# Kernel tuning notes

Measured on AMD Instinct MI355X. Metric: run time of the kernel, lower is better.

Reference implementation:

```python
import jax, jax.numpy as jnp
import numpy as np

IN_CHANNELS = 8
CHANNELS = 8
MASK_OUT_STRIDE = 4
N_IMGS, H, W = 2, 128, 192
N_INST = 256
WEIGHT_NUMS = [(IN_CHANNELS + 2) * CHANNELS, CHANNELS * CHANNELS, CHANNELS * 1]  # [80, 64, 8]
BIAS_NUMS = [CHANNELS, CHANNELS, 1]
NUM_GEN_PARAMS = sum(WEIGHT_NUMS) + sum(BIAS_NUMS)  # 169


def setup_inputs() -> dict:
    key = jax.random.key(0)
    k1, k2, k3, k4, k5 = jax.random.split(key, 5)
    mask_feats = jax.random.normal(k1, (N_IMGS, IN_CHANNELS, H, W), dtype=jnp.float32)
    mask_head_params = jax.random.normal(k2, (N_INST, NUM_GEN_PARAMS), dtype=jnp.float32) * 0.1
    # instance center locations in image coordinates (stride-8 map covers 1024x1536 px)
    instance_locations = jax.random.uniform(k3, (N_INST, 2), dtype=jnp.float32) * jnp.array([W * 8.0, H * 8.0])
    soi = jnp.array([64.0, 128.0, 256.0, 512.0, 1024.0], dtype=jnp.float32)
    im_inds = jax.random.randint(k4, (N_INST,), 0, N_IMGS, dtype=jnp.int32)
    fpn_levels = jax.random.randint(k5, (N_INST,), 0, 5, dtype=jnp.int32)
    return {
        "mask_feats": mask_feats,
        "mask_head_params": mask_head_params,
        "instance_locations": instance_locations,
        "soi": soi,
        "im_inds": im_inds,
        "fpn_levels": fpn_levels,
        "mask_feat_stride": 8,
    }


def compute_locations(h, w, stride):
    shifts_x = jnp.arange(w, dtype=jnp.float32) * stride + stride // 2
    shifts_y = jnp.arange(h, dtype=jnp.float32) * stride + stride // 2
    ys, xs = jnp.meshgrid(shifts_y, shifts_x, indexing="ij")
    return jnp.stack([xs.ravel(), ys.ravel()], axis=1)  # [H*W, 2] (x, y)


def _interp_axis(x, size_in, factor, axis):
    # align_corners=True resize from (size_in+1) samples to (size_in*factor+1):
    # src coordinate of output i is exactly i / factor.
    idx = jnp.arange(size_in * factor + 1)
    i0 = idx // factor
    frac = ((idx % factor).astype(x.dtype)) / factor
    a = jnp.take(x, i0, axis=axis)
    b = jnp.take(x, jnp.minimum(i0 + 1, size_in), axis=axis)
    shape = [1] * x.ndim
    shape[axis] = -1
    f = frac.reshape(shape)
    return a * (1 - f) + b * f


def aligned_bilinear(t, factor):
    # Faithful to AdelaiDet aligned_bilinear: replicate-pad (0,1,0,1), bilinear
    # align_corners=True to (h*f+1, w*f+1), replicate-pad (f//2, 0) top/left, crop.
    if factor == 1:
        return t
    n, c, h, w = t.shape
    t = jnp.pad(t, ((0, 0), (0, 0), (0, 1), (0, 1)), mode="edge")
    t = _interp_axis(t, h, factor, 2)
    t = _interp_axis(t, w, factor, 3)
    p = factor // 2
    t = jnp.pad(t, ((0, 0), (0, 0), (p, 0), (p, 0)), mode="edge")
    return t[:, :, : h * factor, : w * factor]


def reference(mask_feats, mask_head_params, instance_locations, soi, im_inds, fpn_levels, mask_feat_stride):
    n_inst = mask_head_params.shape[0]
    _, c_in, h, w = mask_feats.shape
    hw = h * w

    # relative coordinates, normalized by size-of-interest per FPN level
    locations = compute_locations(h, w, mask_feat_stride)  # [HW, 2]
    rel = instance_locations[:, None, :] - locations[None, :, :]  # [n, HW, 2]
    rel = jnp.transpose(rel, (0, 2, 1))  # [n, 2, HW]
    rel = rel / soi[fpn_levels][:, None, None]
    rel = rel.astype(mask_feats.dtype)

    feats = mask_feats[im_inds].reshape(n_inst, c_in, hw)  # [n, C, HW]
    x = jnp.concatenate([rel, feats], axis=1)  # [n, C+2, HW]

    # parse dynamic params
    splits = np.cumsum(WEIGHT_NUMS + BIAS_NUMS)[:-1]
    w0, w1, w2, b0, b1, b2 = jnp.split(mask_head_params, splits, axis=1)
    w0 = w0.reshape(n_inst, CHANNELS, c_in + 2)
    w1 = w1.reshape(n_inst, CHANNELS, CHANNELS)
    w2 = w2.reshape(n_inst, 1, CHANNELS)

    # grouped 1x1 conv stack == per-instance batched matmul + bias (+ReLU)
    x = jax.nn.relu(jnp.einsum("noi,nip->nop", w0, x) + b0[:, :, None])
    x = jax.nn.relu(jnp.einsum("noi,nip->nop", w1, x) + b1[:, :, None])
    x = jnp.einsum("noi,nip->nop", w2, x) + b2[:, :, None]  # [n, 1, HW]

    logits = x.reshape(n_inst, 1, h, w)
    factor = mask_feat_stride // MASK_OUT_STRIDE
    return aligned_bilinear(logits, factor)  # [n, 1, h*factor, w*factor]
```

## Files before the change

kernel.cpp:

```cpp
#include <hip/hip_runtime.h>


#define HI 128
#define WI 192
#define HW_ (HI * WI)
#define NP 169
#define NOUT_W 384
#define NOUT_H 256
#define LOGITS_BYTES (256u * (unsigned)HW_ * 4u)

__global__ __launch_bounds__(256, 4) void mlp_kernel(
    const float* __restrict__ feats,
    const float* __restrict__ params,
    const float* __restrict__ locs,
    const float* __restrict__ soi,
    const int*   __restrict__ im_inds,
    const int*   __restrict__ lvls,
    float*       __restrict__ logits)
{
    const int b     = blockIdx.x;
    const int n     = b / 24;
    const int chunk = b - n * 24;
    const int t     = threadIdx.x;
    const int p     = chunk * 1024 + (t << 2);

    const int   im    = im_inds[n];
    const float s     = soi[lvls[n]];
    const float inv_s = 1.0f / s;
    const float* __restrict__ P = params + n * NP;
    const float* __restrict__ F = feats + im * (8 * HW_);

    const float step = 8.0f * inv_s;
    const float ax   = (locs[2 * n + 0] - 4.0f) * inv_s;
    const float ay   = (locs[2 * n + 1] - 4.0f) * inv_s;

    const int py  = p / WI;
    const int px0 = p - py * WI;
    const float ry  = ay - (float)py * step;
    const float rx0 = ax - (float)px0 * step;
    const float rx[4] = {rx0, rx0 - step, rx0 - 2.0f * step, rx0 - 3.0f * step};

    float fv[8][4];
    #pragma unroll
    for (int k = 0; k < 8; ++k) {
        const float4 v = *reinterpret_cast<const float4*>(F + k * HW_ + p);
        fv[k][0] = v.x; fv[k][1] = v.y; fv[k][2] = v.z; fv[k][3] = v.w;
    }

    float h0[8][4];
    #pragma unroll
    for (int o = 0; o < 8; ++o) {
        const float base = fmaf(P[o * 10 + 1], ry, P[152 + o]);
        const float wx   = P[o * 10 + 0];
        #pragma unroll
        for (int j = 0; j < 4; ++j) h0[o][j] = fmaf(wx, rx[j], base);
        #pragma unroll
        for (int k = 0; k < 8; ++k) {
            const float w = P[o * 10 + 2 + k];
            #pragma unroll
            for (int j = 0; j < 4; ++j) h0[o][j] = fmaf(w, fv[k][j], h0[o][j]);
        }
        #pragma unroll
        for (int j = 0; j < 4; ++j) h0[o][j] = fmaxf(h0[o][j], 0.0f);
    }

    float h1[8][4];
    #pragma unroll
    for (int o = 0; o < 8; ++o) {
        const float bb = P[160 + o];
        #pragma unroll
        for (int j = 0; j < 4; ++j) h1[o][j] = bb;
        #pragma unroll
        for (int i = 0; i < 8; ++i) {
            const float w = P[80 + o * 8 + i];
            #pragma unroll
            for (int j = 0; j < 4; ++j) h1[o][j] = fmaf(w, h0[i][j], h1[o][j]);
        }
        #pragma unroll
        for (int j = 0; j < 4; ++j) h1[o][j] = fmaxf(h1[o][j], 0.0f);
    }

    float lg[4];
    const float b2 = P[168];
    #pragma unroll
    for (int j = 0; j < 4; ++j) lg[j] = b2;
    #pragma unroll
    for (int i = 0; i < 8; ++i) {
        const float w = P[144 + i];
        #pragma unroll
        for (int j = 0; j < 4; ++j) lg[j] = fmaf(w, h1[i][j], lg[j]);
    }

    float4 st; st.x = lg[0]; st.y = lg[1]; st.z = lg[2]; st.w = lg[3];
    *reinterpret_cast<float4*>(logits + n * HW_ + p) = st;
}

__global__ __launch_bounds__(256, 4) void upsample_kernel(
    const float* __restrict__ logits,
    float*       __restrict__ out)
{
    const int b  = blockIdx.x;
    const int n  = b >> 2;
    const int qq = b & 3;
    const int t  = threadIdx.x;
    const int Y0 = qq << 6;

    const float* __restrict__ Lg = logits + n * HW_;
    float* __restrict__ O = out + n * (NOUT_H * NOUT_W) + Y0 * NOUT_W;

    for (int g = t; g < 3072; g += 256) {
        const int yq = g / 48;
        const int c  = g - yq * 48;
        const int y  = Y0 + yq;
        const int iy2 = (y == 0) ? 0 : (y - 1);
        const int ry0 = iy2 >> 1;
        const int fy  = iy2 & 1;
        const int j0  = c << 2;
        const int jm  = (c == 0) ? 0 : (j0 - 1);

        const float* row0 = Lg + ry0 * WI;
        float4 v  = *reinterpret_cast<const float4*>(row0 + j0);
        float  vm = row0[jm];
        if (fy) {
            const float* row1 = Lg + min(ry0 + 1, HI - 1) * WI;
            const float4 w  = *reinterpret_cast<const float4*>(row1 + j0);
            const float  wm = row1[jm];
            v.x = 0.5f * (v.x + w.x); v.y = 0.5f * (v.y + w.y);
            v.z = 0.5f * (v.z + w.z); v.w = 0.5f * (v.w + w.w);
            vm  = 0.5f * (vm + wm);
        }
        float4 r0, r1;
        r0.x = 0.5f * (vm + v.x);  r0.y = v.x;
        r0.z = 0.5f * (v.x + v.y); r0.w = v.y;
        r1.x = 0.5f * (v.y + v.z); r1.y = v.z;
        r1.z = 0.5f * (v.z + v.w); r1.w = v.w;

        float* o8 = O + (g << 3);
        *reinterpret_cast<float4*>(o8)     = r0;
        *reinterpret_cast<float4*>(o8 + 4) = r1;
    }
}

__global__ __launch_bounds__(512, 4) void dynmask_fused(
    const float* __restrict__ feats, const float* __restrict__ params,
    const float* __restrict__ locs, const float* __restrict__ soi,
    const int* __restrict__ im_inds, const int* __restrict__ lvls,
    float* __restrict__ out)
{
    __shared__ __align__(16) float L[33 * WI];
    const int b  = blockIdx.x;
    const int n  = b >> 2;
    const int qq = b & 3;
    const int t  = threadIdx.x;
    const int R0 = (qq == 0) ? 0 : (32 * qq - 1);

    const int   im    = im_inds[n];
    const float s     = soi[lvls[n]];
    const float inv_s = 1.0f / s;
    const float* __restrict__ P = params + n * NP;
    const float* __restrict__ F = feats + im * (8 * HW_);
    const float step = 8.0f * inv_s;
    const float ax   = (locs[2 * n + 0] - 4.0f) * inv_s;
    const float ay   = (locs[2 * n + 1] - 4.0f) * inv_s;

    for (int idx = t; idx < 3168; idx += 512) {
        const int r   = idx / 96;
        const int c2  = idx - r * 96;
        const int py  = R0 + r;
        const int px0 = c2 * 2;
        const int gp  = py * WI + px0;
        const float ry  = ay - (float)py * step;
        const float rx0 = ax - (float)px0 * step;
        const float rx[2] = {rx0, rx0 - step};

        float fv[8][2];
        #pragma unroll
        for (int k = 0; k < 8; ++k) {
            const float2 v = *reinterpret_cast<const float2*>(F + k * HW_ + gp);
            fv[k][0] = v.x; fv[k][1] = v.y;
        }
        float h0[8][2];
        #pragma unroll
        for (int o = 0; o < 8; ++o) {
            const float base = fmaf(P[o * 10 + 1], ry, P[152 + o]);
            #pragma unroll
            for (int j = 0; j < 2; ++j) h0[o][j] = fmaf(P[o * 10 + 0], rx[j], base);
            #pragma unroll
            for (int k = 0; k < 8; ++k)
                #pragma unroll
                for (int j = 0; j < 2; ++j) h0[o][j] = fmaf(P[o * 10 + 2 + k], fv[k][j], h0[o][j]);
            #pragma unroll
            for (int j = 0; j < 2; ++j) h0[o][j] = fmaxf(h0[o][j], 0.0f);
        }
        float h1[8][2];
        #pragma unroll
        for (int o = 0; o < 8; ++o) {
            #pragma unroll
            for (int j = 0; j < 2; ++j) h1[o][j] = P[160 + o];
            #pragma unroll
            for (int i = 0; i < 8; ++i)
                #pragma unroll
                for (int j = 0; j < 2; ++j) h1[o][j] = fmaf(P[80 + o * 8 + i], h0[i][j], h1[o][j]);
            #pragma unroll
            for (int j = 0; j < 2; ++j) h1[o][j] = fmaxf(h1[o][j], 0.0f);
        }
        float lg[2] = {P[168], P[168]};
        #pragma unroll
        for (int i = 0; i < 8; ++i)
            #pragma unroll
            for (int j = 0; j < 2; ++j) lg[j] = fmaf(P[144 + i], h1[i][j], lg[j]);
        L[idx * 2] = lg[0]; L[idx * 2 + 1] = lg[1];
    }
    __syncthreads();

    const int Y0 = qq << 6;
    float* __restrict__ O = out + n * (NOUT_H * NOUT_W) + Y0 * NOUT_W;
    for (int g = t; g < 3072; g += 512) {
        const int yq = g / 48;
        const int c  = g - yq * 48;
        const int y  = Y0 + yq;
        const int iy2 = (y == 0) ? 0 : (y - 1);
        const int ry0 = iy2 >> 1;
        const int fy  = iy2 & 1;
        const int lr0 = ry0 - R0;
        const int j0  = c << 2;
        const int jm  = (c == 0) ? 0 : (j0 - 1);
        const float* row0 = &L[lr0 * WI];
        float4 v  = *reinterpret_cast<const float4*>(row0 + j0);
        float  vm = row0[jm];
        if (fy) {
            const float* row1 = &L[(min(ry0 + 1, HI - 1) - R0) * WI];
            const float4 w  = *reinterpret_cast<const float4*>(row1 + j0);
            const float  wm = row1[jm];
            v.x = 0.5f * (v.x + w.x); v.y = 0.5f * (v.y + w.y);
            v.z = 0.5f * (v.z + w.z); v.w = 0.5f * (v.w + w.w);
            vm  = 0.5f * (vm + wm);
        }
        float4 r0, r1;
        r0.x = 0.5f * (vm + v.x);  r0.y = v.x;
        r0.z = 0.5f * (v.x + v.y); r0.w = v.y;
        r1.x = 0.5f * (v.y + v.z); r1.y = v.z;
        r1.z = 0.5f * (v.z + v.w); r1.w = v.w;
        float* o8 = O + (g << 3);
        *reinterpret_cast<float4*>(o8)     = r0;
        *reinterpret_cast<float4*>(o8 + 4) = r1;
    }
}

extern "C" void kernel_launch(void* const* d_in, const int* in_sizes, int n_in,
                              void* d_out, int out_size, void* d_ws, size_t ws_size,
                              hipStream_t stream) {
    const float* feats   = (const float*)d_in[0];
    const float* params  = (const float*)d_in[1];
    const float* locs    = (const float*)d_in[2];
    const float* soi     = (const float*)d_in[3];
    const int*   im_inds = (const int*)d_in[4];
    const int*   lvls    = (const int*)d_in[5];
    float*       out     = (float*)d_out;

    if (ws_size >= (size_t)LOGITS_BYTES) {
        float* logits = (float*)d_ws;
        mlp_kernel<<<6144, 256, 0, stream>>>(feats, params, locs, soi, im_inds, lvls, logits);
        upsample_kernel<<<1024, 256, 0, stream>>>(logits, out);
    } else {
        dynmask_fused<<<1024, 512, 0, stream>>>(feats, params, locs, soi, im_inds, lvls, out);
    }
}
```

Measured before the change: 154.3 us.

## Run per-instance dynamic MLP on fp16 MFMA instructions instead of scalar FMAs

Replaces the scalar fp32 FMA implementation of the three-layer per-instance 1x1 conv stack with 16x16x16 fp16 MFMA calls. Biases are folded in as an extra constant-one input row, and a shuffle repacks the outputs before they are stored. This aims to cut the ALU cost of the MLP stage. In exchange it lowers precision to fp16 and replaces vectorized float4 feature loads with scalar per-lane loads, which may leave the stage limited by memory instead.

Measured after the change: 178.8 us. 15.9% more time.

```diff
diff --git a/kernel.cpp b/kernel.cpp
--- a/kernel.cpp
+++ b/kernel.cpp
@@ -9,7 +9,10 @@
 #define NOUT_H 256
 #define LOGITS_BYTES (256u * (unsigned)HW_ * 4u)
 
-__global__ __launch_bounds__(256, 4) void mlp_kernel(
+typedef _Float16 h4 __attribute__((ext_vector_type(4)));
+typedef float    f4 __attribute__((ext_vector_type(4)));
+
+__global__ __launch_bounds__(256, 4) void mlp_mfma_kernel(
     const float* __restrict__ feats,
     const float* __restrict__ params,
     const float* __restrict__ locs,
@@ -18,81 +21,97 @@
     const int*   __restrict__ lvls,
     float*       __restrict__ logits)
 {
-    const int b     = blockIdx.x;
-    const int n     = b / 24;
-    const int chunk = b - n * 24;
-    const int t     = threadIdx.x;
-    const int p     = chunk * 1024 + (t << 2);
-
-    const int   im    = im_inds[n];
-    const float s     = soi[lvls[n]];
+    const int b      = blockIdx.x;
+    const int n_inst = b / 24;
+    const int chunk  = b - n_inst * 24;
+    const int t      = threadIdx.x;
+    const int wave   = t >> 6;
+    const int lane   = t & 63;
+    const int g      = lane >> 4;
+    const int nn     = lane & 15;
+
+    const int   im    = im_inds[n_inst];
+    const float s     = soi[lvls[n_inst]];
     const float inv_s = 1.0f / s;
-    const float* __restrict__ P = params + n * NP;
+    const float* __restrict__ P = params + n_inst * NP;
     const float* __restrict__ F = feats + im * (8 * HW_);
-
     const float step = 8.0f * inv_s;
-    const float ax   = (locs[2 * n + 0] - 4.0f) * inv_s;
-    const float ay   = (locs[2 * n + 1] - 4.0f) * inv_s;
-
-    const int py  = p / WI;
-    const int px0 = p - py * WI;
-    const float ry  = ay - (float)py * step;
-    const float rx0 = ax - (float)px0 * step;
-    const float rx[4] = {rx0, rx0 - step, rx0 - 2.0f * step, rx0 - 3.0f * step};
-
-    float fv[8][4];
+    const float ax   = (locs[2 * n_inst + 0] - 4.0f) * inv_s;
+    const float ay   = (locs[2 * n_inst + 1] - 4.0f) * inv_s;
+
+    h4 A0, A1, A2;
     #pragma unroll
-    for (int k = 0; k < 8; ++k) {
-        const float4 v = *reinterpret_cast<const float4*>(F + k * HW_ + p);
-        fv[k][0] = v.x; fv[k][1] = v.y; fv[k][2] = v.z; fv[k][3] = v.w;
-    }
-
-    float h0[8][4];
-    #pragma unroll
-    for (int o = 0; o < 8; ++o) {
-        const float base = fmaf(P[o * 10 + 1], ry, P[152 + o]);
-        const float wx   = P[o * 10 + 0];
-        #pragma unroll
-        for (int j = 0; j < 4; ++j) h0[o][j] = fmaf(wx, rx[j], base);
-        #pragma unroll
-        for (int k = 0; k < 8; ++k) {
-            const float w = P[o * 10 + 2 + k];
-            #pragma unroll
-            for (int j = 0; j < 4; ++j) h0[o][j] = fmaf(w, fv[k][j], h0[o][j]);
-        }
-        #pragma unroll
-        for (int j = 0; j < 4; ++j) h0[o][j] = fmaxf(h0[o][j], 0.0f);
-    }
-
-    float h1[8][4];
-    #pragma unroll
-    for (int o = 0; o < 8; ++o) {
-        const float bb = P[160 + o];
-        #pragma unroll
-        for (int j = 0; j < 4; ++j) h1[o][j] = bb;
-        #pragma unroll
-        for (int i = 0; i < 8; ++i) {
-            const float w = P[80 + o * 8 + i];
-            #pragma unroll
-            for (int j = 0; j < 4; ++j) h1[o][j] = fmaf(w, h0[i][j], h1[o][j]);
-        }
-        #pragma unroll
-        for (int j = 0; j < 4; ++j) h1[o][j] = fmaxf(h1[o][j], 0.0f);
-    }
-
-    float lg[4];
-    const float b2 = P[168];
-    #pragma unroll
-    for (int j = 0; j < 4; ++j) lg[j] = b2;
-    #pragma unroll
-    for (int i = 0; i < 8; ++i) {
-        const float w = P[144 + i];
-        #pragma unroll
-        for (int j = 0; j < 4; ++j) lg[j] = fmaf(w, h1[i][j], lg[j]);
-    }
-
-    float4 st; st.x = lg[0]; st.y = lg[1]; st.z = lg[2]; st.w = lg[3];
-    *reinterpret_cast<float4*>(logits + n * HW_ + p) = st;
+    for (int j = 0; j < 4; ++j) {
+        const int k = 4 * g + j;
+        float w0 = 0.0f, w1 = 0.0f, w2 = 0.0f;
+        if (nn < 8) {
+            if (k < 10)      w0 = P[nn * 10 + k];
+            else if (k == 10) w0 = P[152 + nn];
+            if (k < 8)       w1 = P[80 + nn * 8 + k];
+            else if (k == 8)  w1 = P[160 + nn];
+        }
+        if (nn == 0) {
+            if (k < 8)       w2 = P[144 + k];
+            else if (k == 8)  w2 = P[168];
+        }
+        A0[j] = (_Float16)w0; A1[j] = (_Float16)w1; A2[j] = (_Float16)w2;
+    }
+
+    const int px_wave = chunk * 1024 + wave * 256;
+    const f4 zero = {0.0f, 0.0f, 0.0f, 0.0f};
+
+    for (int grp = 0; grp < 4; ++grp) {
+        float lgt[4];
+        #pragma unroll
+        for (int tt = 0; tt < 4; ++tt) {
+            const int px0 = px_wave + grp * 64 + tt * 16;
+            const int py  = px0 / WI;
+            const int pxx = px0 - py * WI;
+            const float ry = ay - (float)py * step;
+            const float rx = ax - (float)(pxx + nn) * step;
+            const int   px = px0 + nn;
+
+            h4 B;
+            #pragma unroll
+            for (int j = 0; j < 4; ++j) {
+                const int k = 4 * g + j;
+                const int c = min(max(k - 2, 0), 7);
+                float v = F[c * HW_ + px];
+                v = (k == 0)  ? rx   : v;
+                v = (k == 1)  ? ry   : v;
+                v = (k == 10) ? 1.0f : v;
+                v = (k > 10)  ? 0.0f : v;
+                B[j] = (_Float16)v;
+            }
+
+            f4 C0 = __builtin_amdgcn_mfma_f32_16x16x16f16(A0, B, zero, 0, 0, 0);
+
+            h4 B1;
+            #pragma unroll
+            for (int j = 0; j < 4; ++j) {
+                float r = fmaxf(C0[j], 0.0f);
+                r = (g == 2) ? ((j == 0) ? 1.0f : 0.0f) : r;
+                B1[j] = (_Float16)r;
+            }
+            f4 C1 = __builtin_amdgcn_mfma_f32_16x16x16f16(A1, B1, zero, 0, 0, 0);
+
+            h4 B2;
+            #pragma unroll
+            for (int j = 0; j < 4; ++j) {
+                float r = fmaxf(C1[j], 0.0f);
+                r = (g == 2) ? ((j == 0) ? 1.0f : 0.0f) : r;
+                B2[j] = (_Float16)r;
+            }
+            f4 C2 = __builtin_amdgcn_mfma_f32_16x16x16f16(A2, B2, zero, 0, 0, 0);
+            lgt[tt] = C2[0];
+        }
+        const float v0 = __shfl(lgt[0], nn, 64);
+        const float v1 = __shfl(lgt[1], nn, 64);
+        const float v2 = __shfl(lgt[2], nn, 64);
+        const float v3 = __shfl(lgt[3], nn, 64);
+        float outv = (g == 0) ? v0 : (g == 1) ? v1 : (g == 2) ? v2 : v3;
+        logits[n_inst * HW_ + px_wave + grp * 64 + lane] = outv;
+    }
 }
 
 __global__ __launch_bounds__(256, 4) void upsample_kernel(
@@ -260,7 +279,7 @@
 
     if (ws_size >= (size_t)LOGITS_BYTES) {
         float* logits = (float*)d_ws;
-        mlp_kernel<<<6144, 256, 0, stream>>>(feats, params, locs, soi, im_inds, lvls, logits);
+        mlp_mfma_kernel<<<6144, 256, 0, stream>>>(feats, params, locs, soi, im_inds, lvls, logits);
         upsample_kernel<<<1024, 256, 0, stream>>>(logits, out);
     } else {
         dynmask_fused<<<1024, 512, 0, stream>>>(feats, params, locs, soi, im_inds, lvls, out);
```
